# Performance work log

Measured on AMD Instinct MI355X. Metric: run time of the kernel, lower is better.

The kernel has to match this reference:

```python
import jax, jax.numpy as jnp
import numpy as np

B, C, H, P, G = 512, 64, 128, 16, 2  # batch, in_dim, hidden_dim, num_prompts, num_groups
EPS = 1e-5


def _layernorm(v, w, b):
    mu = jnp.mean(v, axis=-1, keepdims=True)
    var = jnp.var(v, axis=-1, keepdims=True)
    return (v - mu) * jax.lax.rsqrt(var + EPS) * w + b


def setup_inputs() -> dict:
    key = jax.random.key(0)
    ks = jax.random.split(key, 8)
    def xavier(k, shape):
        fan_in, fan_out = shape[-2], shape[-1]
        lim = float(np.sqrt(6.0 / (fan_in + fan_out)))
        return jax.random.uniform(k, shape, jnp.float32, -lim, lim)
    return {
        "x": jax.random.normal(ks[0], (B, C, H), jnp.float32),
        "x_prompt": jax.random.normal(ks[1], (B, P, H), jnp.float32),
        "emb_column": xavier(ks[2], (C, H)),
        "emb_prompt": xavier(ks[3], (P, H)),
        "lin_w": xavier(ks[4], (H, 2 * H)),  # torch Linear weight [out, in]
        "lin_b": jnp.zeros((H,), jnp.float32),
        "ln_col_w": jnp.ones((H,), jnp.float32),
        "ln_col_b": jnp.zeros((H,), jnp.float32),
        "ln_pr_w": jnp.ones((H,), jnp.float32),
        "ln_pr_b": jnp.zeros((H,), jnp.float32),
        "expand_weight": jax.random.uniform(ks[5], (P,), jnp.float32),
        "gn_w": jnp.ones((P,), jnp.float32),
        "gn_b": jnp.zeros((P,), jnp.float32),
    }


def reference(x, x_prompt, emb_column, emb_prompt, lin_w, lin_b,
              ln_col_w, ln_col_b, ln_pr_w, ln_pr_b,
              expand_weight, gn_w, gn_b):
    ec = _layernorm(emb_column, ln_col_w, ln_col_b)          # [C,H]
    ep = _layernorm(emb_prompt, ln_pr_w, ln_pr_b)            # [P,H]
    se_prompt = jnp.broadcast_to(ep, (x.shape[0], P, H))     # [B,P,H]
    cat = jnp.concatenate([se_prompt, x_prompt], axis=-1)    # [B,P,2H]
    hat = jnp.einsum('bpk,hk->bph', cat, lin_w) + lin_b + se_prompt + x_prompt
    m = jnp.einsum('bph,ch->bpc', hat, ec)                   # [B,P,C]
    m = jax.nn.softmax(m, axis=-1)
    # outer-product expansion + relu: [B,P,C,H]
    xe = jax.nn.relu(jnp.einsum('bch,p->bpch', x, expand_weight))
    # GroupNorm over channels P (groups G), stats over (P/G, C, H)
    xg = xe.reshape(x.shape[0], G, P // G, C, H)
    mu = jnp.mean(xg, axis=(2, 3, 4), keepdims=True)
    var = jnp.var(xg, axis=(2, 3, 4), keepdims=True)
    xg = (xg - mu) * jax.lax.rsqrt(var + EPS)
    xn = xg.reshape(x.shape[0], P, C, H) * gn_w[:, None, None] + gn_b[:, None, None]
    xn = xn + x[:, None, :, :]                               # residual
    return jnp.einsum('bpch,bpc->bph', xn, m)                # weighted reduce over C
```

## Files before the change

### kernel.cpp

```cpp
#include <hip/hip_runtime.h>

#define B_ 512
#define C_ 64
#define H_ 128
#define P_ 16
#define G_ 2
#define EPS 1e-5f

#define XS_S 130
#define HB_S 136
#define MB_S 72

typedef __attribute__((ext_vector_type(8))) short bf16x8;
typedef __attribute__((ext_vector_type(4))) float f32x4;

__device__ __forceinline__ unsigned short f2bf(float f) {
    union { float f; unsigned u; } v; v.f = f;
    return (unsigned short)((v.u + 0x7FFFu + ((v.u >> 16) & 1u)) >> 16);
}
__device__ __forceinline__ float bf2f(unsigned short h) {
    union { unsigned u; float f; } v; v.u = ((unsigned)h) << 16; return v.f;
}
__device__ __forceinline__ unsigned packbf(float lo, float hi) {
    return (unsigned)f2bf(lo) | ((unsigned)f2bf(hi) << 16);
}
__device__ __forceinline__ void split2(float a, float b, unsigned& hi, unsigned& lo) {
    const unsigned short ah = f2bf(a), bh = f2bf(b);
    const unsigned short al = f2bf(a - bf2f(ah)), bl = f2bf(b - bf2f(bh));
    hi = (unsigned)ah | ((unsigned)bh << 16);
    lo = (unsigned)al | ((unsigned)bl << 16);
}
__device__ __forceinline__ bf16x8 relu8(bf16x8 x) {
    union { bf16x8 v; unsigned u[4]; } a; a.v = x;
    #pragma unroll
    for (int i = 0; i < 4; ++i) {
        unsigned s = a.u[i] & 0x80008000u;
        a.u[i] &= ~((s >> 15) * 0xFFFFu);
    }
    return a.v;
}

__global__ __launch_bounds__(256) void prep_kernel(
    const float* __restrict__ emb_column,
    const float* __restrict__ emb_prompt,
    const float* __restrict__ lin_w,
    const float* __restrict__ lin_b,
    const float* __restrict__ ln_col_w, const float* __restrict__ ln_col_b,
    const float* __restrict__ ln_pr_w,  const float* __restrict__ ln_pr_b,
    float* __restrict__ hat0,
    unsigned short* __restrict__ ec_hi,
    unsigned short* __restrict__ ec_lo,
    unsigned short* __restrict__ w2_hi,
    unsigned short* __restrict__ w2_lo)
{
    __shared__ __align__(16) float ep_s[P_ * H_];
    const int t = threadIdx.x;
    const int blk = blockIdx.x;

    {
        const int r = t >> 4, j = t & 15;
        float v[8]; float s = 0.f, s2 = 0.f;
        #pragma unroll
        for (int i = 0; i < 8; ++i) {
            v[i] = emb_prompt[r * H_ + j + 16 * i];
            s += v[i]; s2 += v[i] * v[i];
        }
        #pragma unroll
        for (int m = 1; m < 16; m <<= 1) { s += __shfl_xor(s, m, 64); s2 += __shfl_xor(s2, m, 64); }
        const float mean = s * (1.f / H_);
        const float rs = rsqrtf(s2 * (1.f / H_) - mean * mean + EPS);
        #pragma unroll
        for (int i = 0; i < 8; ++i) {
            const int h = j + 16 * i;
            ep_s[r * H_ + h] = (v[i] - mean) * rs * ln_pr_w[h] + ln_pr_b[h];
        }
    }
    {
        const int r = blk * 8 + (t >> 5), j = t & 31;
        float v[4]; float s = 0.f, s2 = 0.f;
        #pragma unroll
        for (int i = 0; i < 4; ++i) {
            v[i] = emb_column[r * H_ + j + 32 * i];
            s += v[i]; s2 += v[i] * v[i];
        }
        #pragma unroll
        for (int m = 1; m < 32; m <<= 1) { s += __shfl_xor(s, m, 64); s2 += __shfl_xor(s2, m, 64); }
        const float mean = s * (1.f / H_);
        const float rs = rsqrtf(s2 * (1.f / H_) - mean * mean + EPS);
        #pragma unroll
        for (int i = 0; i < 4; ++i) {
            const int h = j + 32 * i;
            const float val = (v[i] - mean) * rs * ln_col_w[h] + ln_col_b[h];
            const unsigned short hi = f2bf(val);
            ec_hi[r * H_ + h] = hi;
            ec_lo[r * H_ + h] = f2bf(val - bf2f(hi));
        }
    }
    {
        const int flat = blk * 2048 + t * 8;
        const int h = flat >> 7, k0 = flat & 127;
        const float4* src = (const float4*)(lin_w + h * (2 * H_) + H_ + k0);
        const float4 q0 = src[0], q1 = src[1];
        uint4 ph, pl;
        split2(q0.x, q0.y, ph.x, pl.x);
        split2(q0.z, q0.w, ph.y, pl.y);
        split2(q1.x, q1.y, ph.z, pl.z);
        split2(q1.z, q1.w, ph.w, pl.w);
        *(uint4*)(w2_hi + flat) = ph;
        *(uint4*)(w2_lo + flat) = pl;
    }
    __syncthreads();
    {
        const int p = blk * 2 + (t >> 7);
        const int h = t & 127;
        float acc = lin_b[h] + ep_s[p * H_ + h];
        const float4* w1 = (const float4*)(lin_w + h * (2 * H_));
        const float4* e4 = (const float4*)(ep_s + p * H_);
        for (int k = 0; k < H_ / 4; ++k) {
            const float4 w = w1[k]; const float4 e = e4[k];
            acc += e.x * w.x + e.y * w.y + e.z * w.z + e.w * w.w;
        }
        hat0[p * H_ + h] = acc;
    }
}

__global__ __launch_bounds__(256) void main_kernel(
    const float* __restrict__ x,
    const float* __restrict__ x_prompt,
    const float* __restrict__ expand_w,
    const float* __restrict__ gn_w, const float* __restrict__ gn_b,
    const float* __restrict__ hat0,
    const unsigned short* __restrict__ ec_hi,
    const unsigned short* __restrict__ ec_lo,
    const unsigned short* __restrict__ w2_hi,
    const unsigned short* __restrict__ w2_lo,
    float* __restrict__ out)
{
    __shared__ __align__(16) unsigned short xs_bf[C_ * XS_S];
    __shared__ __align__(16) unsigned short xp_hi[P_ * HB_S];
    __shared__ __align__(16) unsigned short xp_lo[P_ * HB_S];
    __shared__ __align__(16) unsigned short hat_hi[P_ * HB_S];
    __shared__ __align__(16) unsigned short hat_lo[P_ * HB_S];
    __shared__ __align__(16) float sm[P_ * C_];
    __shared__ __align__(16) unsigned short m_bf[P_ * MB_S];
    __shared__ float red[16];
    __shared__ float stat[4];
    __shared__ float s1_s[P_], s2_s[P_];
    __shared__ float cA[P_], cB[P_], cD[P_];

    const int t = threadIdx.x;
    const int b = blockIdx.x;
    const int lane = t & 63;
    const int w = t >> 6;
    const int nl = lane & 15;
    const int quad = lane >> 4;

    {
        const float4* x4 = (const float4*)(x + (size_t)b * (C_ * H_));
        float xsum = 0.f, xsq = 0.f, r1 = 0.f, r2 = 0.f;
        #pragma unroll
        for (int i = 0; i < 8; ++i) {
            const int idx = t + 256 * i;
            const float4 v = x4[idx];
            const int c = idx >> 5;
            const int h0 = (idx & 31) * 4;
            unsigned* dst = (unsigned*)(xs_bf + c * XS_S + h0);
            dst[0] = packbf(v.x, v.y);
            dst[1] = packbf(v.z, v.w);
            xsum += (v.x + v.y) + (v.z + v.w);
            xsq  += (v.x * v.x + v.y * v.y) + (v.z * v.z + v.w * v.w);
            const float rx = fmaxf(v.x, 0.f), ry = fmaxf(v.y, 0.f);
            const float rz = fmaxf(v.z, 0.f), rw = fmaxf(v.w, 0.f);
            r1 += (rx + ry) + (rz + rw);
            r2 += (rx * rx + ry * ry) + (rz * rz + rw * rw);
        }
        #pragma unroll
        for (int m = 1; m < 64; m <<= 1) {
            xsum += __shfl_xor(xsum, m, 64);
            xsq  += __shfl_xor(xsq,  m, 64);
            r1   += __shfl_xor(r1,   m, 64);
            r2   += __shfl_xor(r2,   m, 64);
        }
        if (lane == 0) {
            red[w * 4 + 0] = xsum; red[w * 4 + 1] = xsq;
            red[w * 4 + 2] = r1;   red[w * 4 + 3] = r2;
        }
        const float4* xp4 = (const float4*)(x_prompt + (size_t)b * (P_ * H_));
        const float4 a0 = xp4[2 * t], a1 = xp4[2 * t + 1];
        const int p = t >> 4, hh = (t & 15) * 8;
        uint4 ph, pl;
        split2(a0.x, a0.y, ph.x, pl.x);
        split2(a0.z, a0.w, ph.y, pl.y);
        split2(a1.x, a1.y, ph.z, pl.z);
        split2(a1.z, a1.w, ph.w, pl.w);
        *(uint4*)(xp_hi + p * HB_S + hh) = ph;
        *(uint4*)(xp_lo + p * HB_S + hh) = pl;
    }
    __syncthreads();
    if (t < 4) stat[t] = red[t] + red[4 + t] + red[8 + t] + red[12 + t];

    {
        f32x4 acc[2] = {{0.f,0.f,0.f,0.f},{0.f,0.f,0.f,0.f}};
        #pragma unroll
        for (int kk = 0; kk < 4; ++kk) {
            const bf16x8 a_hi = *(const bf16x8*)(xp_hi + nl * HB_S + kk * 32 + quad * 8);
            const bf16x8 a_lo = *(const bf16x8*)(xp_lo + nl * HB_S + kk * 32 + quad * 8);
            #pragma unroll
            for (int T = 0; T < 2; ++T) {
                const int h = w * 32 + T * 16 + nl;
                const bf16x8 b_hi = *(const bf16x8*)(w2_hi + h * H_ + kk * 32 + quad * 8);
                const bf16x8 b_lo = *(const bf16x8*)(w2_lo + h * H_ + kk * 32 + quad * 8);
                acc[T] = __builtin_amdgcn_mfma_f32_16x16x32_bf16(a_hi, b_hi, acc[T], 0, 0, 0);
                acc[T] = __builtin_amdgcn_mfma_f32_16x16x32_bf16(a_lo, b_hi, acc[T], 0, 0, 0);
                acc[T] = __builtin_amdgcn_mfma_f32_16x16x32_bf16(a_hi, b_lo, acc[T], 0, 0, 0);
            }
        }
        const float* xpg = x_prompt + (size_t)b * (P_ * H_);
        #pragma unroll
        for (int T = 0; T < 2; ++T) {
            const int h = w * 32 + T * 16 + nl;
            #pragma unroll
            for (int r = 0; r < 4; ++r) {
                const int p = quad * 4 + r;
                const float val = acc[T][r] + hat0[p * H_ + h] + xpg[p * H_ + h];
                const unsigned short hi = f2bf(val);
                hat_hi[p * HB_S + h] = hi;
                hat_lo[p * HB_S + h] = f2bf(val - bf2f(hi));
            }
        }
    }
    __syncthreads();

    if (t < P_) {
        const float ew = expand_w[t];
        const float Ap = fabsf(ew);
        const float Bp = fminf(ew, 0.f);
        s1_s[t] = Ap * stat[2] + Bp * stat[0];
        s2_s[t] = ew * ew * (ew >= 0.f ? stat[3] : (stat[1] - stat[3]));
    }
    {
        f32x4 acc = {0.f, 0.f, 0.f, 0.f};
        const int c = w * 16 + nl;
        #pragma unroll
        for (int kk = 0; kk < 4; ++kk) {
            const bf16x8 a_hi = *(const bf16x8*)(hat_hi + nl * HB_S + kk * 32 + quad * 8);
            const bf16x8 a_lo = *(const bf16x8*)(hat_lo + nl * HB_S + kk * 32 + quad * 8);
            const bf16x8 b_hi = *(const bf16x8*)(ec_hi + c * H_ + kk * 32 + quad * 8);
            const bf16x8 b_lo = *(const bf16x8*)(ec_lo + c * H_ + kk * 32 + quad * 8);
            acc = __builtin_amdgcn_mfma_f32_16x16x32_bf16(a_hi, b_hi, acc, 0, 0, 0);
            acc = __builtin_amdgcn_mfma_f32_16x16x32_bf16(a_lo, b_hi, acc, 0, 0, 0);
            acc = __builtin_amdgcn_mfma_f32_16x16x32_bf16(a_hi, b_lo, acc, 0, 0, 0);
        }
        #pragma unroll
        for (int r = 0; r < 4; ++r) sm[(quad * 4 + r) * C_ + c] = acc[r];
    }
    __syncthreads();

    if (t < P_) {
        const int g = t >> 3;
        float S1 = 0.f, S2 = 0.f;
        #pragma unroll
        for (int q = 0; q < 8; ++q) { S1 += s1_s[g * 8 + q]; S2 += s2_s[g * 8 + q]; }
        const float invN = 1.f / (float)((P_ / G_) * C_ * H_);
        const float mu = S1 * invN;
        const float var = S2 * invN - mu * mu;
        const float rs = rsqrtf(var + EPS);
        const float a = rs * gn_w[t];
        const float ew = expand_w[t];
        cA[t] = a * fabsf(ew);
        cB[t] = a * fminf(ew, 0.f) + 1.f;
        cD[t] = gn_b[t] - mu * a;
    }
    {
        const int p = t >> 4, j = t & 15;
        float v0 = sm[p * C_ + j],      v1 = sm[p * C_ + j + 16];
        float v2 = sm[p * C_ + j + 32], v3 = sm[p * C_ + j + 48];
        float mx = fmaxf(fmaxf(v0, v1), fmaxf(v2, v3));
        #pragma unroll
        for (int m = 1; m < 16; m <<= 1) mx = fmaxf(mx, __shfl_xor(mx, m, 64));
        const float e0 = __expf(v0 - mx), e1 = __expf(v1 - mx);
        const float e2 = __expf(v2 - mx), e3 = __expf(v3 - mx);
        float ssum = (e0 + e1) + (e2 + e3);
        #pragma unroll
        for (int m = 1; m < 16; m <<= 1) ssum += __shfl_xor(ssum, m, 64);
        const float inv = 1.f / ssum;
        m_bf[p * MB_S + j]      = f2bf(e0 * inv);
        m_bf[p * MB_S + j + 16] = f2bf(e1 * inv);
        m_bf[p * MB_S + j + 32] = f2bf(e2 * inv);
        m_bf[p * MB_S + j + 48] = f2bf(e3 * inv);
    }
    __syncthreads();

    {
        f32x4 aU[2] = {{0.f,0.f,0.f,0.f},{0.f,0.f,0.f,0.f}};
        f32x4 aT[2] = {{0.f,0.f,0.f,0.f},{0.f,0.f,0.f,0.f}};
        #pragma unroll
        for (int kk = 0; kk < 2; ++kk) {
            const bf16x8 af = *(const bf16x8*)(m_bf + nl * MB_S + kk * 32 + quad * 8);
            #pragma unroll
            for (int T = 0; T < 2; ++T) {
                const int h = w * 32 + T * 16 + nl;
                union { bf16x8 v; unsigned short s[8]; } bu;
                const int c0 = kk * 32 + quad * 8;
                #pragma unroll
                for (int j = 0; j < 8; ++j) bu.s[j] = xs_bf[(c0 + j) * XS_S + h];
                aU[T] = __builtin_amdgcn_mfma_f32_16x16x32_bf16(af, bu.v, aU[T], 0, 0, 0);
                const bf16x8 br = relu8(bu.v);
                aT[T] = __builtin_amdgcn_mfma_f32_16x16x32_bf16(af, br, aT[T], 0, 0, 0);
            }
        }
        float* ob = out + (size_t)b * (P_ * H_);
        #pragma unroll
        for (int T = 0; T < 2; ++T) {
            const int h = w * 32 + T * 16 + nl;
            #pragma unroll
            for (int r = 0; r < 4; ++r) {
                const int p = quad * 4 + r;
                ob[p * H_ + h] = cA[p] * aT[T][r] + cB[p] * aU[T][r] + cD[p];
            }
        }
    }
}

extern "C" void kernel_launch(void* const* d_in, const int* in_sizes, int n_in,
                              void* d_out, int out_size, void* d_ws, size_t ws_size,
                              hipStream_t stream) {
    const float* x          = (const float*)d_in[0];
    const float* x_prompt   = (const float*)d_in[1];
    const float* emb_column = (const float*)d_in[2];
    const float* emb_prompt = (const float*)d_in[3];
    const float* lin_w      = (const float*)d_in[4];
    const float* lin_b      = (const float*)d_in[5];
    const float* ln_col_w   = (const float*)d_in[6];
    const float* ln_col_b   = (const float*)d_in[7];
    const float* ln_pr_w    = (const float*)d_in[8];
    const float* ln_pr_b    = (const float*)d_in[9];
    const float* expand_w   = (const float*)d_in[10];
    const float* gn_w       = (const float*)d_in[11];
    const float* gn_b       = (const float*)d_in[12];
    float* out = (float*)d_out;

    float* hat0 = (float*)d_ws;
    unsigned short* ec_hi = (unsigned short*)(hat0 + P_ * H_);
    unsigned short* ec_lo = ec_hi + C_ * H_;
    unsigned short* w2_hi = ec_lo + C_ * H_;
    unsigned short* w2_lo = w2_hi + H_ * H_;

    prep_kernel<<<8, 256, 0, stream>>>(emb_column, emb_prompt, lin_w, lin_b,
                                       ln_col_w, ln_col_b, ln_pr_w, ln_pr_b,
                                       hat0, ec_hi, ec_lo, w2_hi, w2_lo);
    main_kernel<<<B_, 256, 0, stream>>>(x, x_prompt, expand_w, gn_w, gn_b,
                                        hat0, ec_hi, ec_lo, w2_hi, w2_lo, out);
}
```

Baseline: 103.3 us.

## Spread prep kernel across 64 blocks, prefetch hat0/x_prompt, cheaper bf16 pack

Splits the prep kernel into 64 blocks with distinct roles: 16 blocks each layer-normalize one prompt row and compute its hat0 row, 16 blocks normalize column embeddings, and 32 blocks split the lin_w half into hi/lo bf16. This removes the redundant per-block prompt layernorm and the serial 128-thread dot loop. The main kernel now loads hat0 and x_prompt into registers at the start, so their latency overlaps the x load. It also switches the x-to-bf16 pack to round-half-up without ties-to-even, which changes rounding slightly and adds register pressure.

```diff
diff --git a/kernel.cpp b/kernel.cpp
--- a/kernel.cpp
+++ b/kernel.cpp
@@ -21,8 +21,9 @@
 __device__ __forceinline__ float bf2f(unsigned short h) {
     union { unsigned u; float f; } v; v.u = ((unsigned)h) << 16; return v.f;
 }
-__device__ __forceinline__ unsigned packbf(float lo, float hi) {
-    return (unsigned)f2bf(lo) | ((unsigned)f2bf(hi) << 16);
+__device__ __forceinline__ unsigned packbf_fast(float lo, float hi) {
+    union { float f; unsigned u; } a, b; a.f = lo; b.f = hi;
+    return ((a.u + 0x8000u) >> 16) | (((b.u + 0x8000u) >> 16) << 16);
 }
 __device__ __forceinline__ void split2(float a, float b, unsigned& hi, unsigned& lo) {
     const unsigned short ah = f2bf(a), bh = f2bf(b);
@@ -53,74 +54,62 @@
     unsigned short* __restrict__ w2_hi,
     unsigned short* __restrict__ w2_lo)
 {
-    __shared__ __align__(16) float ep_s[P_ * H_];
+    __shared__ __align__(16) float ep_row[H_];
     const int t = threadIdx.x;
     const int blk = blockIdx.x;
-
-    {
-        const int r = t >> 4, j = t & 15;
-        float v[8]; float s = 0.f, s2 = 0.f;
-        #pragma unroll
-        for (int i = 0; i < 8; ++i) {
-            v[i] = emb_prompt[r * H_ + j + 16 * i];
-            s += v[i]; s2 += v[i] * v[i];
-        }
-        #pragma unroll
-        for (int m = 1; m < 16; m <<= 1) { s += __shfl_xor(s, m, 64); s2 += __shfl_xor(s2, m, 64); }
+    const int lane = t & 63;
+    const int w = t >> 6;
+
+    if (blk < 16) {
+        const int p = blk;
+        const float v0 = emb_prompt[p * H_ + lane];
+        const float v1 = emb_prompt[p * H_ + lane + 64];
+        float s = v0 + v1, s2 = v0 * v0 + v1 * v1;
+        #pragma unroll
+        for (int m = 1; m < 64; m <<= 1) { s += __shfl_xor(s, m, 64); s2 += __shfl_xor(s2, m, 64); }
         const float mean = s * (1.f / H_);
         const float rs = rsqrtf(s2 * (1.f / H_) - mean * mean + EPS);
-        #pragma unroll
-        for (int i = 0; i < 8; ++i) {
-            const int h = j + 16 * i;
-            ep_s[r * H_ + h] = (v[i] - mean) * rs * ln_pr_w[h] + ln_pr_b[h];
-        }
-    }
-    {
-        const int r = blk * 8 + (t >> 5), j = t & 31;
-        float v[4]; float s = 0.f, s2 = 0.f;
-        #pragma unroll
-        for (int i = 0; i < 4; ++i) {
-            v[i] = emb_column[r * H_ + j + 32 * i];
-            s += v[i]; s2 += v[i] * v[i];
-        }
-        #pragma unroll
-        for (int m = 1; m < 32; m <<= 1) { s += __shfl_xor(s, m, 64); s2 += __shfl_xor(s2, m, 64); }
+        if (w == 0) {
+            ep_row[lane]      = (v0 - mean) * rs * ln_pr_w[lane]      + ln_pr_b[lane];
+            ep_row[lane + 64] = (v1 - mean) * rs * ln_pr_w[lane + 64] + ln_pr_b[lane + 64];
+        }
+        __syncthreads();
+        const int h = t >> 1;
+        const int kh = (t & 1) * 16;
+        const float4* w1 = (const float4*)(lin_w + h * (2 * H_)) + kh;
+        const float4* e4 = (const float4*)ep_row + kh;
+        float acc = 0.f;
+        #pragma unroll
+        for (int k = 0; k < 16; ++k) {
+            const float4 W = w1[k], E = e4[k];
+            acc += E.x * W.x + E.y * W.y + E.z * W.z + E.w * W.w;
+        }
+        acc += __shfl_xor(acc, 1, 64);
+        if ((t & 1) == 0) hat0[p * H_ + h] = acc + lin_b[h] + ep_row[h];
+    } else if (blk < 32) {
+        const int r = (blk - 16) * 4 + w;
+        const float v0 = emb_column[r * H_ + lane];
+        const float v1 = emb_column[r * H_ + lane + 64];
+        float s = v0 + v1, s2 = v0 * v0 + v1 * v1;
+        #pragma unroll
+        for (int m = 1; m < 64; m <<= 1) { s += __shfl_xor(s, m, 64); s2 += __shfl_xor(s2, m, 64); }
         const float mean = s * (1.f / H_);
         const float rs = rsqrtf(s2 * (1.f / H_) - mean * mean + EPS);
-        #pragma unroll
-        for (int i = 0; i < 4; ++i) {
-            const int h = j + 32 * i;
-            const float val = (v[i] - mean) * rs * ln_col_w[h] + ln_col_b[h];
-            const unsigned short hi = f2bf(val);
-            ec_hi[r * H_ + h] = hi;
-            ec_lo[r * H_ + h] = f2bf(val - bf2f(hi));
-        }
-    }
-    {
-        const int flat = blk * 2048 + t * 8;
-        const int h = flat >> 7, k0 = flat & 127;
-        const float4* src = (const float4*)(lin_w + h * (2 * H_) + H_ + k0);
-        const float4 q0 = src[0], q1 = src[1];
-        uint4 ph, pl;
-        split2(q0.x, q0.y, ph.x, pl.x);
-        split2(q0.z, q0.w, ph.y, pl.y);
-        split2(q1.x, q1.y, ph.z, pl.z);
-        split2(q1.z, q1.w, ph.w, pl.w);
-        *(uint4*)(w2_hi + flat) = ph;
-        *(uint4*)(w2_lo + flat) = pl;
-    }
-    __syncthreads();
-    {
-        const int p = blk * 2 + (t >> 7);
-        const int h = t & 127;
-        float acc = lin_b[h] + ep_s[p * H_ + h];
-        const float4* w1 = (const float4*)(lin_w + h * (2 * H_));
-        const float4* e4 = (const float4*)(ep_s + p * H_);
-        for (int k = 0; k < H_ / 4; ++k) {
-            const float4 w = w1[k]; const float4 e = e4[k];
-            acc += e.x * w.x + e.y * w.y + e.z * w.z + e.w * w.w;
-        }
-        hat0[p * H_ + h] = acc;
+        const float a0 = (v0 - mean) * rs * ln_col_w[lane]      + ln_col_b[lane];
+        const float a1 = (v1 - mean) * rs * ln_col_w[lane + 64] + ln_col_b[lane + 64];
+        const unsigned short h0 = f2bf(a0), h1 = f2bf(a1);
+        ec_hi[r * H_ + lane]      = h0;
+        ec_hi[r * H_ + lane + 64] = h1;
+        ec_lo[r * H_ + lane]      = f2bf(a0 - bf2f(h0));
+        ec_lo[r * H_ + lane + 64] = f2bf(a1 - bf2f(h1));
+    } else {
+        const int f = (blk - 32) * 512 + t * 2;
+        const int h = f >> 7, k = f & 127;
+        const float2 q = *(const float2*)(lin_w + h * (2 * H_) + H_ + k);
+        unsigned hi, lo;
+        split2(q.x, q.y, hi, lo);
+        *(unsigned*)(w2_hi + f) = hi;
+        *(unsigned*)(w2_lo + f) = lo;
     }
 }
 
@@ -155,6 +144,21 @@
     const int nl = lane & 15;
     const int quad = lane >> 4;
 
+    float h0r[2][4], xpr[2][4];
+    {
+        const float* xpg = x_prompt + (size_t)b * (P_ * H_);
+        #pragma unroll
+        for (int T = 0; T < 2; ++T) {
+            const int h = w * 32 + T * 16 + nl;
+            #pragma unroll
+            for (int r = 0; r < 4; ++r) {
+                const int p = quad * 4 + r;
+                h0r[T][r] = hat0[p * H_ + h];
+                xpr[T][r] = xpg[p * H_ + h];
+            }
+        }
+    }
+
     {
         const float4* x4 = (const float4*)(x + (size_t)b * (C_ * H_));
         float xsum = 0.f, xsq = 0.f, r1 = 0.f, r2 = 0.f;
@@ -165,8 +169,8 @@
             const int c = idx >> 5;
             const int h0 = (idx & 31) * 4;
             unsigned* dst = (unsigned*)(xs_bf + c * XS_S + h0);
-            dst[0] = packbf(v.x, v.y);
-            dst[1] = packbf(v.z, v.w);
+            dst[0] = packbf_fast(v.x, v.y);
+            dst[1] = packbf_fast(v.z, v.w);
             xsum += (v.x + v.y) + (v.z + v.w);
             xsq  += (v.x * v.x + v.y * v.y) + (v.z * v.z + v.w * v.w);
             const float rx = fmaxf(v.x, 0.f), ry = fmaxf(v.y, 0.f);
@@ -215,14 +219,13 @@
                 acc[T] = __builtin_amdgcn_mfma_f32_16x16x32_bf16(a_hi, b_lo, acc[T], 0, 0, 0);
             }
         }
-        const float* xpg = x_prompt + (size_t)b * (P_ * H_);
         #pragma unroll
         for (int T = 0; T < 2; ++T) {
             const int h = w * 32 + T * 16 + nl;
             #pragma unroll
             for (int r = 0; r < 4; ++r) {
                 const int p = quad * 4 + r;
-                const float val = acc[T][r] + hat0[p * H_ + h] + xpg[p * H_ + h];
+                const float val = acc[T][r] + h0r[T][r] + xpr[T][r];
                 const unsigned short hi = f2bf(val);
                 hat_hi[p * HB_S + h] = hi;
                 hat_lo[p * HB_S + h] = f2bf(val - bf2f(hi));
@@ -346,9 +349,9 @@
     unsigned short* w2_hi = ec_lo + C_ * H_;
     unsigned short* w2_lo = w2_hi + H_ * H_;
 
-    prep_kernel<<<8, 256, 0, stream>>>(emb_column, emb_prompt, lin_w, lin_b,
-                                       ln_col_w, ln_col_b, ln_pr_w, ln_pr_b,
-                                       hat0, ec_hi, ec_lo, w2_hi, w2_lo);
+    prep_kernel<<<64, 256, 0, stream>>>(emb_column, emb_prompt, lin_w, lin_b,
+                                        ln_col_w, ln_col_b, ln_pr_w, ln_pr_b,
+                                        hat0, ec_hi, ec_lo, w2_hi, w2_lo);
     main_kernel<<<B_, 256, 0, stream>>>(x, x_prompt, expand_w, gn_w, gn_b,
                                         hat0, ec_hi, ec_lo, w2_hi, w2_lo, out);
 }
```

Measured after the change: 100.8 us. 1.02x faster.
